# Optimization experiments

Measured on AMD Instinct MI355X. Metric: run time of the kernel, lower is better.

Reference implementation:

```python
import jax, jax.numpy as jnp
import numpy as np

NU, NI, F, H, D = 100000, 50000, 256, 8, 64
E1, E2 = 300000, 300000
SLOPE = 0.2  # DGL GATConv default negative_slope


def setup_inputs() -> dict:
    key = jax.random.key(0)
    ks = jax.random.split(key, 20)
    p = lambda k, sh: jax.random.normal(k, sh, jnp.float32) * 0.1
    return {
        "h_user": jax.random.normal(ks[0], (NU, F), jnp.float32),
        "h_item": jax.random.normal(ks[1], (NI, F), jnp.float32),
        "src_u2i": jax.random.randint(ks[2], (E1,), 0, NU),
        "dst_u2i": jax.random.randint(ks[3], (E1,), 0, NI),
        "src_i2u": jax.random.randint(ks[4], (E2,), 0, NI),
        "dst_i2u": jax.random.randint(ks[5], (E2,), 0, NU),
        "W_src_u2i": p(ks[6], (F, H * D)), "W_dst_u2i": p(ks[7], (F, H * D)),
        "al_u2i": p(ks[8], (H, D)), "ar_u2i": p(ks[9], (H, D)),
        "bias_u2i": jnp.zeros((H * D,), jnp.float32), "W_res_u2i": p(ks[10], (F, H * D)),
        "W_src_i2u": p(ks[11], (F, H * D)), "W_dst_i2u": p(ks[12], (F, H * D)),
        "al_i2u": p(ks[13], (H, D)), "ar_i2u": p(ks[14], (H, D)),
        "bias_i2u": jnp.zeros((H * D,), jnp.float32), "W_res_i2u": p(ks[15], (F, H * D)),
    }


def _gat(h_src, h_dst, src, dst, Ws, Wd, al, ar, b, Wr, n_dst):
    # linear projections -> [N, H, D]
    fs = (h_src @ Ws).reshape(-1, H, D)
    fd = (h_dst @ Wd).reshape(-1, H, D)
    el = jnp.einsum('nhd,hd->nh', fs, al)   # a_l . Wh_src
    er = jnp.einsum('nhd,hd->nh', fd, ar)   # a_r . Wh_dst
    e = jax.nn.leaky_relu(el[src] + er[dst], SLOPE)  # [E, H]
    # segment softmax over incoming edges of each dst node
    m = jax.ops.segment_max(e, dst, num_segments=n_dst)
    m = jnp.where(jnp.isfinite(m), m, jnp.float32(0))  # nodes with no edges
    ex = jnp.exp(e - m[dst])
    s = jax.ops.segment_sum(ex, dst, num_segments=n_dst)
    a = ex / s[dst]                                   # [E, H]
    # weighted scatter-sum of gathered source features
    out = jax.ops.segment_sum(a[:, :, None] * fs[src], dst, num_segments=n_dst)
    res = (h_dst @ Wr).reshape(-1, H, D)              # residual projection
    return out + res + b.reshape(1, H, D)


def reference(h_user, h_item, src_u2i, dst_u2i, src_i2u, dst_i2u,
              W_src_u2i, W_dst_u2i, al_u2i, ar_u2i, bias_u2i, W_res_u2i,
              W_src_i2u, W_dst_i2u, al_i2u, ar_i2u, bias_i2u, W_res_i2u):
    out_item = _gat(h_user, h_item, src_u2i, dst_u2i,
                    W_src_u2i, W_dst_u2i, al_u2i, ar_u2i, bias_u2i, W_res_u2i, NI)
    out_user = _gat(h_item, h_user, src_i2u, dst_i2u,
                    W_src_i2u, W_dst_i2u, al_i2u, ar_i2u, bias_i2u, W_res_i2u, NU)
    return (out_user, out_item)
```

## Files before the change

### kernel.cpp

```cpp
#include <hip/hip_runtime.h>
#include <cstdint>
#include <cstddef>

#define NU_ 100000
#define NI_ 50000
#define F_ 256
#define H_ 8
#define HD_ 512
#define NE_ 300000
#define SLOPE_ 0.2f

#define MPAD_U 100096
#define MPAD_I 50048
#define MT_U (MPAD_U / 128)
#define MT_I (MPAD_I / 128)
#define GEMM_NB ((MT_U + MT_I) * 4)

#define SCAN_N (NI_ + NU_)
#define SCAN_CHUNK 2048
#define SCAN_NB ((SCAN_N + SCAN_CHUNK - 1) / SCAN_CHUNK)

#define PREP_COPY_U (NU_ * F_ / 2048)
#define PREP_COPY_I (NI_ * F_ / 2048)
#define PREP_COPY (PREP_COPY_U + PREP_COPY_I)
#define PREP_WCONV 2048
#define PREP_FOLD 32
#define PREP_HIST ((2 * NE_ + 255) / 256)
#define PREP_NB (PREP_COPY + PREP_WCONV + PREP_FOLD + PREP_HIST)

typedef float f32x4 __attribute__((ext_vector_type(4)));
typedef __bf16 bf16x8 __attribute__((ext_vector_type(8)));
typedef unsigned short u16x8 __attribute__((ext_vector_type(8)));
typedef unsigned short u16x4 __attribute__((ext_vector_type(4)));

static __device__ __forceinline__ unsigned short f2bf_bits(float f) {
  unsigned u = __float_as_uint(f);
  u += 0x7fffu + ((u >> 16) & 1u);
  return (unsigned short)(u >> 16);
}
static __device__ __forceinline__ float bf2f(unsigned short b) {
  return __uint_as_float(((unsigned)b) << 16);
}
static __device__ __forceinline__ unsigned cvt_pk_bf16(float lo, float hi) {
  unsigned r;
  asm("v_cvt_pk_bf16_f32 %0, %1, %2" : "=v"(r) : "v"(lo), "v"(hi));
  return r;
}

#define GLL16(g, l)                                                        \
  __builtin_amdgcn_global_load_lds(                                        \
      (const __attribute__((address_space(1))) void*)(g),                  \
      (__attribute__((address_space(3))) void*)(l), 16, 0, 0)

__global__ __launch_bounds__(256) void prep_kernel(const float* __restrict__ h_user,
                                                   const float* __restrict__ h_item,
                                                   const float* __restrict__ W0,
                                                   const float* __restrict__ W1,
                                                   const float* __restrict__ W2,
                                                   const float* __restrict__ W3,
                                                   const float* __restrict__ Wd0,
                                                   const float* __restrict__ Wd1,
                                                   const float* __restrict__ a0,
                                                   const float* __restrict__ a1,
                                                   const float* __restrict__ a2,
                                                   const float* __restrict__ a3,
                                                   const int* __restrict__ dst_u2i,
                                                   const int* __restrict__ dst_i2u,
                                                   unsigned short* __restrict__ hb_user,
                                                   unsigned short* __restrict__ hb_item,
                                                   unsigned short* __restrict__ Wt,
                                                   unsigned short* __restrict__ wfb,
                                                   int* __restrict__ deg) {
  int bid = blockIdx.x;
  if (bid < PREP_COPY) {
    bool user = bid < PREP_COPY_U;
    const float* h = user ? h_user : h_item;
    unsigned short* hb = user ? hb_user : hb_item;
    size_t base = (size_t)(user ? bid : bid - PREP_COPY_U) * 2048 + threadIdx.x * 8;
    f32x4 a = *(const f32x4*)&h[base];
    f32x4 b = *(const f32x4*)&h[base + 4];
    u16x8 o;
    o[0] = f2bf_bits(a.x); o[1] = f2bf_bits(a.y); o[2] = f2bf_bits(a.z); o[3] = f2bf_bits(a.w);
    o[4] = f2bf_bits(b.x); o[5] = f2bf_bits(b.y); o[6] = f2bf_bits(b.z); o[7] = f2bf_bits(b.w);
    *(u16x8*)&hb[base] = o;
  } else if (bid < PREP_COPY + PREP_WCONV) {
    int idx = (bid - PREP_COPY) * 256 + threadIdx.x;
    int m = idx >> 17;
    int r = idx & 131071;
    const float* W = (m == 0) ? W0 : (m == 1) ? W1 : (m == 2) ? W2 : W3;
    int f = r & 255, c = r >> 8;
    Wt[idx] = f2bf_bits(W[(size_t)f * HD_ + c]);
  } else if (bid < PREP_COPY + PREP_WCONV + PREP_FOLD) {
    int b = bid - PREP_COPY - PREP_WCONV;
    int m = b >> 3;
    int idx = (b & 7) * 256 + threadIdx.x;
    const float* W = (m == 0) ? W0 : (m == 1) ? Wd0 : (m == 2) ? W2 : Wd1;
    const float* av = (m == 0) ? a0 : (m == 1) ? a1 : (m == 2) ? a2 : a3;
    int f = idx & 255, hh = idx >> 8;
    float acc = 0.f;
#pragma unroll 8
    for (int d = 0; d < 64; ++d) acc += W[(size_t)f * HD_ + hh * 64 + d] * av[hh * 64 + d];
    int buf = (m == 0 || m == 3) ? 0 : 1;
    int rowoff = (m == 1 || m == 3) ? 8 : 0;
    wfb[buf * 4096 + (rowoff + hh) * 256 + f] = f2bf_bits(acc);
  } else {
    int e = (bid - PREP_COPY - PREP_WCONV - PREP_FOLD) * 256 + threadIdx.x;
    if (e < NE_) atomicAdd(&deg[dst_u2i[e]], 1);
    else if (e < 2 * NE_) atomicAdd(&deg[NI_ + dst_i2u[e - NE_]], 1);
  }
}

__global__ __launch_bounds__(256) void gemm2_kernel(const unsigned short* __restrict__ hb_user,
                                                    const unsigned short* __restrict__ hb_item,
                                                    const unsigned short* __restrict__ Wt,
                                                    const unsigned short* __restrict__ wfb,
                                                    unsigned short* __restrict__ fs_u2i,
                                                    unsigned short* __restrict__ fs_i2u,
                                                    unsigned short* __restrict__ res_user,
                                                    unsigned short* __restrict__ res_item,
                                                    const float* __restrict__ bias_u2i,
                                                    const float* __restrict__ bias_i2u,
                                                    float* __restrict__ el_u2i,
                                                    float* __restrict__ er_i2u,
                                                    float* __restrict__ el_i2u,
                                                    float* __restrict__ er_u2i,
                                                    const int* __restrict__ deg,
                                                    int* __restrict__ bsum) {
  __shared__ unsigned short lds[2][3][128][32];
  if (blockIdx.x >= GEMM_NB) {
    int* ilds = (int*)&lds[0][0][0][0];
    int tid = threadIdx.x;
    int base = (blockIdx.x - GEMM_NB) * SCAN_CHUNK + tid * 8;
    int sum = 0;
#pragma unroll
    for (int j = 0; j < 8; ++j) sum += (base + j < SCAN_N) ? deg[base + j] : 0;
    ilds[tid] = sum;
    __syncthreads();
    for (int o = 128; o > 0; o >>= 1) {
      if (tid < o) ilds[tid] += ilds[tid + o];
      __syncthreads();
    }
    if (tid == 0) bsum[blockIdx.x - GEMM_NB] = ilds[0];
    return;
  }
  int bid;
  {
    constexpr int qq = GEMM_NB / 8, rr = GEMM_NB % 8;
    int xcd = blockIdx.x & 7, sidx = blockIdx.x >> 3;
    bid = (xcd < rr ? xcd * (qq + 1) : rr * (qq + 1) + (xcd - rr) * qq) + sidx;
  }
  bool user = bid < MT_U * 4;
  if (!user) bid -= MT_U * 4;
  const unsigned short* Ab  = user ? hb_user : hb_item;
  const unsigned short* B1t = user ? (Wt + 0 * HD_ * F_) : (Wt + 2 * HD_ * F_);
  const unsigned short* B2t = user ? (Wt + 3 * HD_ * F_) : (Wt + 1 * HD_ * F_);
  const unsigned short* wfs = user ? wfb : (wfb + 4096);
  unsigned short* fs  = user ? fs_u2i : fs_i2u;
  unsigned short* res = user ? res_user : res_item;
  const float* bias = user ? bias_i2u : bias_u2i;
  int M = user ? NU_ : NI_;

  int tid = threadIdx.x;
  int lane = tid & 63;
  int wave = tid >> 6;
  int wm = wave >> 1, wn = wave & 1;
  int mt = bid >> 2, nt = bid & 3;
  int bm = mt * 128, bn = nt * 128;
  f32x4 acc1[4][4] = {};
  f32x4 acc2[4][4] = {};
  f32x4 acc3[4] = {};
  int lr = lane & 15;
  int kk = (lane >> 4) * 8;
  int ksw = ((lane >> 4) ^ ((lr >> 1) & 3)) << 3;

  int r0 = tid >> 2;
  int c0 = (tid & 3) << 3;
  int cs = (((tid & 3) ^ ((r0 >> 1) & 3)) << 3);
  const unsigned short* gA  = &Ab [(size_t)(bm + r0) * 256 + cs];
  const unsigned short* gB1 = &B1t[(size_t)(bn + r0) * 256 + cs];
  const unsigned short* gB2 = &B2t[(size_t)(bn + r0) * 256 + cs];

  bf16x8 b3f[8];
  if (nt == 0) {
#pragma unroll
    for (int t = 0; t < 8; ++t)
      b3f[t] = __builtin_bit_cast(bf16x8, *(const u16x8*)&wfs[(size_t)lr * 256 + kk + t * 32]);
  }

#define STAGE(buf, t)                                                       \
  do {                                                                      \
    int k0_ = (t) * 32;                                                     \
    GLL16(gA  + k0_,          &lds[buf][0][r0][c0]);                        \
    GLL16(gA  + k0_ + 64*256, &lds[buf][0][r0 + 64][c0]);                   \
    GLL16(gB1 + k0_,          &lds[buf][1][r0][c0]);                        \
    GLL16(gB1 + k0_ + 64*256, &lds[buf][1][r0 + 64][c0]);                   \
    GLL16(gB2 + k0_,          &lds[buf][2][r0][c0]);                        \
    GLL16(gB2 + k0_ + 64*256, &lds[buf][2][r0 + 64][c0]);                   \
  } while (0)

  STAGE(0, 0);
#pragma unroll
  for (int t = 0; t < 8; ++t) {
    if (t < 7) STAGE((t + 1) & 1, t + 1);
    if (t < 7) asm volatile("s_waitcnt vmcnt(6)" ::: "memory");
    else       asm volatile("s_waitcnt vmcnt(0)" ::: "memory");
    __builtin_amdgcn_s_barrier();
    __builtin_amdgcn_sched_barrier(0);
    const int cb = t & 1;
    bf16x8 af[4], b1[4], b2[4];
#pragma unroll
    for (int m = 0; m < 4; ++m)
      af[m] = __builtin_bit_cast(bf16x8, *(const u16x8*)&lds[cb][0][wm * 64 + m * 16 + lr][ksw]);
#pragma unroll
    for (int n = 0; n < 4; ++n) {
      b1[n] = __builtin_bit_cast(bf16x8, *(const u16x8*)&lds[cb][1][wn * 64 + n * 16 + lr][ksw]);
      b2[n] = __builtin_bit_cast(bf16x8, *(const u16x8*)&lds[cb][2][wn * 64 + n * 16 + lr][ksw]);
    }
#pragma unroll
    for (int m = 0; m < 4; ++m)
#pragma unroll
      for (int n = 0; n < 4; ++n) {
        acc1[m][n] = __builtin_amdgcn_mfma_f32_16x16x32_bf16(b1[n], af[m], acc1[m][n], 0, 0, 0);
        acc2[m][n] = __builtin_amdgcn_mfma_f32_16x16x32_bf16(b2[n], af[m], acc2[m][n], 0, 0, 0);
      }
    if (nt == 0) {
#pragma unroll
      for (int m = 0; m < 4; ++m)
        acc3[m] = __builtin_amdgcn_mfma_f32_16x16x32_bf16(af[m], b3f[t], acc3[m], 0, 0, 0);
    }
    __builtin_amdgcn_sched_barrier(0);
    __builtin_amdgcn_s_barrier();
  }
#undef STAGE

  int rg = (lane >> 4) * 4;
  f32x4 bsv[4];
#pragma unroll
  for (int n = 0; n < 4; ++n)
    bsv[n] = *(const f32x4*)&bias[bn + wn * 64 + n * 16 + rg];
#pragma unroll
  for (int m = 0; m < 4; ++m) {
    int row = bm + wm * 64 + m * 16 + lr;
    if (row < M) {
#pragma unroll
      for (int n = 0; n < 4; ++n) {
        int col = bn + wn * 64 + n * 16 + rg;
        uint2 v1;
        v1.x = cvt_pk_bf16(acc1[m][n][0], acc1[m][n][1]);
        v1.y = cvt_pk_bf16(acc1[m][n][2], acc1[m][n][3]);
        *(uint2*)&fs[(size_t)row * HD_ + col] = v1;
        uint2 v2;
        v2.x = cvt_pk_bf16(acc2[m][n][0] + bsv[n].x, acc2[m][n][1] + bsv[n].y);
        v2.y = cvt_pk_bf16(acc2[m][n][2] + bsv[n].z, acc2[m][n][3] + bsv[n].w);
        *(uint2*)&res[(size_t)row * HD_ + col] = v2;
      }
    }
  }
  if (nt == 0 && wn == 0) {
    float* elp = user ? el_u2i : el_i2u;
    float* erp = user ? er_i2u : er_u2i;
#pragma unroll
    for (int m = 0; m < 4; ++m) {
#pragma unroll
      for (int r = 0; r < 4; ++r) {
        int row = bm + wm * 64 + m * 16 + rg + r;
        if (row >= M) continue;
        if (lr < 8) elp[(size_t)row * 8 + lr] = acc3[m][r];
        else        erp[(size_t)row * 8 + lr - 8] = acc3[m][r];
      }
    }
  }
}

__global__ __launch_bounds__(256) void scan_apply_kernel(const int* __restrict__ deg,
                                                         const int* __restrict__ bsum,
                                                         int* __restrict__ rowstart,
                                                         int* __restrict__ cursor) {
  __shared__ int sb[128];
  __shared__ int lds[256];
  int tid = threadIdx.x;
  if (tid < 128) sb[tid] = (tid < SCAN_NB) ? bsum[tid] : 0;
  __syncthreads();
  for (int o = 1; o < 128; o <<= 1) {
    int t = (tid < 128 && tid >= o) ? sb[tid - o] : 0;
    __syncthreads();
    if (tid < 128) sb[tid] += t;
    __syncthreads();
  }
  int blockpref = (blockIdx.x == 0) ? 0 : sb[blockIdx.x - 1];
  int base = blockIdx.x * SCAN_CHUNK + tid * 8;
  int v[8];
  int sum = 0;
#pragma unroll
  for (int j = 0; j < 8; ++j) {
    v[j] = (base + j < SCAN_N) ? deg[base + j] : 0;
    sum += v[j];
  }
  lds[tid] = sum;
  __syncthreads();
  for (int o = 1; o < 256; o <<= 1) {
    int t = (tid >= o) ? lds[tid - o] : 0;
    __syncthreads();
    lds[tid] += t;
    __syncthreads();
  }
  int run = blockpref + lds[tid] - sum;
#pragma unroll
  for (int j = 0; j < 8; ++j) {
    if (base + j < SCAN_N) { rowstart[base + j] = run; cursor[base + j] = run; }
    run += v[j];
  }
  if (blockIdx.x == 0 && tid == 0) rowstart[SCAN_N] = 2 * NE_;
}

__global__ __launch_bounds__(256) void bin_kernel(const int* __restrict__ src_u2i,
                                                  const int* __restrict__ dst_u2i,
                                                  const int* __restrict__ src_i2u,
                                                  const int* __restrict__ dst_i2u,
                                                  int* __restrict__ cursor,
                                                  int* __restrict__ ssrc) {
  int e = blockIdx.x * 256 + threadIdx.x;
  int de, se;
  if (e < NE_) { de = dst_u2i[e]; se = src_u2i[e]; }
  else if (e < 2 * NE_) { de = NI_ + dst_i2u[e - NE_]; se = src_i2u[e - NE_]; }
  else return;
  int pos = atomicAdd(&cursor[de], 1);
  ssrc[pos] = se;
}

__global__ __launch_bounds__(256) void accum_kernel(const int* __restrict__ rowstart,
                                                    const int* __restrict__ ssrc,
                                                    const float* __restrict__ el_u2i,
                                                    const float* __restrict__ el_i2u,
                                                    const float* __restrict__ er_u2i,
                                                    const float* __restrict__ er_i2u,
                                                    const unsigned short* __restrict__ fs_u2i,
                                                    const unsigned short* __restrict__ fs_i2u,
                                                    const unsigned short* __restrict__ res_user,
                                                    const unsigned short* __restrict__ res_item,
                                                    float* __restrict__ out_item,
                                                    float* __restrict__ out_user) {
  int n = blockIdx.x * 4 + (threadIdx.x >> 6);
  int lane = threadIdx.x & 63;
  bool item = n < NI_;
  int ln = item ? n : n - NI_;
  const unsigned short* res = item ? res_item : res_user;
  float* out = (item ? out_item : out_user) + (size_t)ln * HD_;
  int r0 = rowstart[n], r1 = rowstart[n + 1];
  float acc[8] = {};
  if (r0 < r1) {
    const float* el = item ? el_u2i : el_i2u;
    const float* er = item ? er_u2i : er_i2u;
    const unsigned short* fs = item ? fs_u2i : fs_i2u;
    int hh = lane >> 3;
    float erh = er[(size_t)ln * 8 + hh];
    float m = -3.0e38f, s = 0.f;
    int k = r0;
    for (; k + 2 <= r1; k += 2) {
      int s0 = ssrc[k], s1 = ssrc[k + 1];
      float e0 = el[(size_t)s0 * 8 + hh] + erh;
      float e1 = el[(size_t)s1 * 8 + hh] + erh;
      e0 = e0 > 0.f ? e0 : SLOPE_ * e0;
      e1 = e1 > 0.f ? e1 : SLOPE_ * e1;
      u16x8 v0 = *(const u16x8*)&fs[(size_t)s0 * HD_ + lane * 8];
      u16x8 v1 = *(const u16x8*)&fs[(size_t)s1 * HD_ + lane * 8];
      float mm = fmaxf(e0, e1);
      if (mm > m) {
        float r = __expf(m - mm);
        s *= r;
#pragma unroll
        for (int j = 0; j < 8; ++j) acc[j] *= r;
        m = mm;
      }
      float x0 = __expf(e0 - m), x1 = __expf(e1 - m);
      s += x0 + x1;
#pragma unroll
      for (int j = 0; j < 8; ++j)
        acc[j] += x0 * bf2f((unsigned short)v0[j]) + x1 * bf2f((unsigned short)v1[j]);
    }
    if (k < r1) {
      int s0 = ssrc[k];
      float e0 = el[(size_t)s0 * 8 + hh] + erh;
      e0 = e0 > 0.f ? e0 : SLOPE_ * e0;
      u16x8 v0 = *(const u16x8*)&fs[(size_t)s0 * HD_ + lane * 8];
      if (e0 > m) {
        float r = __expf(m - e0);
        s *= r;
#pragma unroll
        for (int j = 0; j < 8; ++j) acc[j] *= r;
        m = e0;
      }
      float x0 = __expf(e0 - m);
      s += x0;
#pragma unroll
      for (int j = 0; j < 8; ++j) acc[j] += x0 * bf2f((unsigned short)v0[j]);
    }
    float inv = 1.f / s;
#pragma unroll
    for (int j = 0; j < 8; ++j) acc[j] *= inv;
  }
  u16x8 rv = *(const u16x8*)&res[(size_t)ln * HD_ + lane * 8];
  f32x4 o0, o1;
#pragma unroll
  for (int j = 0; j < 4; ++j) {
    o0[j] = acc[j] + bf2f((unsigned short)rv[j]);
    o1[j] = acc[4 + j] + bf2f((unsigned short)rv[4 + j]);
  }
  float* op = out + lane * 8;
  *(f32x4*)op = o0;
  *(f32x4*)(op + 4) = o1;
}

extern "C" void kernel_launch(void* const* d_in, const int* in_sizes, int n_in,
                              void* d_out, int out_size, void* d_ws, size_t ws_size,
                              hipStream_t stream) {
  const float* h_user    = (const float*)d_in[0];
  const float* h_item    = (const float*)d_in[1];
  const int*   src_u2i   = (const int*)d_in[2];
  const int*   dst_u2i   = (const int*)d_in[3];
  const int*   src_i2u   = (const int*)d_in[4];
  const int*   dst_i2u   = (const int*)d_in[5];
  const float* W_src_u2i = (const float*)d_in[6];
  const float* W_dst_u2i = (const float*)d_in[7];
  const float* al_u2i    = (const float*)d_in[8];
  const float* ar_u2i    = (const float*)d_in[9];
  const float* bias_u2i  = (const float*)d_in[10];
  const float* W_res_u2i = (const float*)d_in[11];
  const float* W_src_i2u = (const float*)d_in[12];
  const float* W_dst_i2u = (const float*)d_in[13];
  const float* al_i2u    = (const float*)d_in[14];
  const float* ar_i2u    = (const float*)d_in[15];
  const float* bias_i2u  = (const float*)d_in[16];
  const float* W_res_i2u = (const float*)d_in[17];

  float* out_user = (float*)d_out;
  float* out_item = (float*)d_out + (size_t)NU_ * HD_;

  char* ws = (char*)d_ws;
  size_t off = 0;
  auto take = [&](size_t bytes) -> char* {
    char* p = ws + off;
    off += (bytes + 255) & ~(size_t)255;
    return p;
  };
  unsigned short* fs_u2i   = (unsigned short*)take((size_t)NU_ * HD_ * 2);
  unsigned short* fs_i2u   = (unsigned short*)take((size_t)NI_ * HD_ * 2);
  unsigned short* res_user = (unsigned short*)take((size_t)NU_ * HD_ * 2);
  unsigned short* res_item = (unsigned short*)take((size_t)NI_ * HD_ * 2);
  unsigned short* hb_user  = (unsigned short*)take((size_t)MPAD_U * F_ * 2);
  unsigned short* hb_item  = (unsigned short*)take((size_t)MPAD_I * F_ * 2);
  unsigned short* Wt  = (unsigned short*)take((size_t)4 * HD_ * F_ * 2);
  unsigned short* wfb = (unsigned short*)take((size_t)2 * 16 * F_ * 2);
  float* el_u2i = (float*)take((size_t)NU_ * 8 * 4);
  float* er_i2u = (float*)take((size_t)NU_ * 8 * 4);
  float* el_i2u = (float*)take((size_t)NI_ * 8 * 4);
  float* er_u2i = (float*)take((size_t)NI_ * 8 * 4);
  int* deg_all      = (int*)take((size_t)SCAN_N * 4);
  int* rowstart_all = (int*)take((size_t)(SCAN_N + 1) * 4);
  int* cursor_all   = (int*)take((size_t)SCAN_N * 4);
  int* bsum         = (int*)take((size_t)128 * 4);
  int* ssrc         = (int*)take((size_t)2 * NE_ * 4);

  hipMemsetAsync(deg_all, 0, (size_t)SCAN_N * 4, stream);

  prep_kernel<<<PREP_NB, 256, 0, stream>>>(h_user, h_item,
                                           W_src_u2i, W_res_u2i, W_src_i2u, W_res_i2u,
                                           W_dst_u2i, W_dst_i2u,
                                           al_u2i, ar_u2i, al_i2u, ar_i2u,
                                           dst_u2i, dst_i2u,
                                           hb_user, hb_item, Wt, wfb, deg_all);

  gemm2_kernel<<<GEMM_NB + SCAN_NB, 256, 0, stream>>>(hb_user, hb_item, Wt, wfb,
                                                      fs_u2i, fs_i2u, res_user, res_item,
                                                      bias_u2i, bias_i2u,
                                                      el_u2i, er_i2u, el_i2u, er_u2i,
                                                      deg_all, bsum);

  scan_apply_kernel<<<SCAN_NB, 256, 0, stream>>>(deg_all, bsum, rowstart_all, cursor_all);
  constexpr int EB2 = (2 * NE_ + 255) / 256;
  bin_kernel<<<EB2, 256, 0, stream>>>(src_u2i, dst_u2i, src_i2u, dst_i2u, cursor_all, ssrc);

  accum_kernel<<<SCAN_N / 4, 256, 0, stream>>>(rowstart_all, ssrc,
                                               el_u2i, el_i2u, er_u2i, er_i2u,
                                               fs_u2i, fs_i2u, res_user, res_item,
                                               out_item, out_user);
}
```

Measured before the change: 498.0 us.

## Split dual-output GEMM into single-output tiles with separate el/er blocks and LDS-staged stores

Each GEMM block previously computed both the source projection and the residual projection for one A tile, with the attention-logit MFMA folded in. Now each block computes one output (fs or res), so there are twice as many blocks. Each block uses two LDS operands instead of three and holds half the accumulators, which should cut register pressure and raise occupancy. The el/er logits move into dedicated blocks that read A directly from global memory, and the epilogue stages bf16 results through padded LDS so the global stores are coalesced 16-byte writes. The cost is that each A tile is loaded twice from memory, plus one more time by the el/er blocks.

Measured after the change: 462.5 us (median of 4 runs). 1.08x faster.

```diff
diff --git a/kernel.cpp b/kernel.cpp
--- a/kernel.cpp
+++ b/kernel.cpp
@@ -14,7 +14,8 @@
 #define MPAD_I 50048
 #define MT_U (MPAD_U / 128)
 #define MT_I (MPAD_I / 128)
-#define GEMM_NB ((MT_U + MT_I) * 4)
+#define NT_ALL ((MT_U + MT_I) * 8)
+#define EL_NB (MT_U + MT_I)
 
 #define SCAN_N (NI_ + NU_)
 #define SCAN_CHUNK 2048
@@ -32,6 +33,7 @@
 typedef __bf16 bf16x8 __attribute__((ext_vector_type(8)));
 typedef unsigned short u16x8 __attribute__((ext_vector_type(8)));
 typedef unsigned short u16x4 __attribute__((ext_vector_type(4)));
+typedef unsigned int u32x4 __attribute__((ext_vector_type(4)));
 
 static __device__ __forceinline__ unsigned short f2bf_bits(float f) {
   unsigned u = __float_as_uint(f);
@@ -110,6 +112,8 @@
   }
 }
 
+#define EPITCH 136
+#define LOFF(b, m, r) ((((b) * 2 + (m)) * 128 + (r)) * 32)
 __global__ __launch_bounds__(256) void gemm2_kernel(const unsigned short* __restrict__ hb_user,
                                                     const unsigned short* __restrict__ hb_item,
                                                     const unsigned short* __restrict__ Wt,
@@ -126,11 +130,16 @@
                                                     float* __restrict__ er_u2i,
                                                     const int* __restrict__ deg,
                                                     int* __restrict__ bsum) {
-  __shared__ unsigned short lds[2][3][128][32];
-  if (blockIdx.x >= GEMM_NB) {
-    int* ilds = (int*)&lds[0][0][0][0];
-    int tid = threadIdx.x;
-    int base = (blockIdx.x - GEMM_NB) * SCAN_CHUNK + tid * 8;
+  __shared__ unsigned short sh[17408];
+  int tid = threadIdx.x;
+  int lane = tid & 63;
+  int wave = tid >> 6;
+  int lr = lane & 15;
+  int kk = (lane >> 4) * 8;
+
+  if (blockIdx.x >= NT_ALL + EL_NB) {
+    int* ilds = (int*)sh;
+    int base = (blockIdx.x - NT_ALL - EL_NB) * SCAN_CHUNK + tid * 8;
     int sum = 0;
 #pragma unroll
     for (int j = 0; j < 8; ++j) sum += (base + j < SCAN_N) ? deg[base + j] : 0;
@@ -140,137 +149,146 @@
       if (tid < o) ilds[tid] += ilds[tid + o];
       __syncthreads();
     }
-    if (tid == 0) bsum[blockIdx.x - GEMM_NB] = ilds[0];
+    if (tid == 0) bsum[blockIdx.x - NT_ALL - EL_NB] = ilds[0];
     return;
   }
-  int bid;
-  {
-    constexpr int qq = GEMM_NB / 8, rr = GEMM_NB % 8;
-    int xcd = blockIdx.x & 7, sidx = blockIdx.x >> 3;
-    bid = (xcd < rr ? xcd * (qq + 1) : rr * (qq + 1) + (xcd - rr) * qq) + sidx;
-  }
-  bool user = bid < MT_U * 4;
-  if (!user) bid -= MT_U * 4;
-  const unsigned short* Ab  = user ? hb_user : hb_item;
-  const unsigned short* B1t = user ? (Wt + 0 * HD_ * F_) : (Wt + 2 * HD_ * F_);
-  const unsigned short* B2t = user ? (Wt + 3 * HD_ * F_) : (Wt + 1 * HD_ * F_);
-  const unsigned short* wfs = user ? wfb : (wfb + 4096);
-  unsigned short* fs  = user ? fs_u2i : fs_i2u;
-  unsigned short* res = user ? res_user : res_item;
-  const float* bias = user ? bias_i2u : bias_u2i;
-  int M = user ? NU_ : NI_;
-
-  int tid = threadIdx.x;
-  int lane = tid & 63;
-  int wave = tid >> 6;
-  int wm = wave >> 1, wn = wave & 1;
-  int mt = bid >> 2, nt = bid & 3;
-  int bm = mt * 128, bn = nt * 128;
-  f32x4 acc1[4][4] = {};
-  f32x4 acc2[4][4] = {};
-  f32x4 acc3[4] = {};
-  int lr = lane & 15;
-  int kk = (lane >> 4) * 8;
-  int ksw = ((lane >> 4) ^ ((lr >> 1) & 3)) << 3;
-
-  int r0 = tid >> 2;
-  int c0 = (tid & 3) << 3;
-  int cs = (((tid & 3) ^ ((r0 >> 1) & 3)) << 3);
-  const unsigned short* gA  = &Ab [(size_t)(bm + r0) * 256 + cs];
-  const unsigned short* gB1 = &B1t[(size_t)(bn + r0) * 256 + cs];
-  const unsigned short* gB2 = &B2t[(size_t)(bn + r0) * 256 + cs];
-
-  bf16x8 b3f[8];
-  if (nt == 0) {
-#pragma unroll
-    for (int t = 0; t < 8; ++t)
-      b3f[t] = __builtin_bit_cast(bf16x8, *(const u16x8*)&wfs[(size_t)lr * 256 + kk + t * 32]);
-  }
-
-#define STAGE(buf, t)                                                       \
-  do {                                                                      \
-    int k0_ = (t) * 32;                                                     \
-    GLL16(gA  + k0_,          &lds[buf][0][r0][c0]);                        \
-    GLL16(gA  + k0_ + 64*256, &lds[buf][0][r0 + 64][c0]);                   \
-    GLL16(gB1 + k0_,          &lds[buf][1][r0][c0]);                        \
-    GLL16(gB1 + k0_ + 64*256, &lds[buf][1][r0 + 64][c0]);                   \
-    GLL16(gB2 + k0_,          &lds[buf][2][r0][c0]);                        \
-    GLL16(gB2 + k0_ + 64*256, &lds[buf][2][r0 + 64][c0]);                   \
-  } while (0)
-
-  STAGE(0, 0);
-#pragma unroll
-  for (int t = 0; t < 8; ++t) {
-    if (t < 7) STAGE((t + 1) & 1, t + 1);
-    if (t < 7) asm volatile("s_waitcnt vmcnt(6)" ::: "memory");
-    else       asm volatile("s_waitcnt vmcnt(0)" ::: "memory");
-    __builtin_amdgcn_s_barrier();
-    __builtin_amdgcn_sched_barrier(0);
-    const int cb = t & 1;
-    bf16x8 af[4], b1[4], b2[4];
-#pragma unroll
-    for (int m = 0; m < 4; ++m)
-      af[m] = __builtin_bit_cast(bf16x8, *(const u16x8*)&lds[cb][0][wm * 64 + m * 16 + lr][ksw]);
-#pragma unroll
-    for (int n = 0; n < 4; ++n) {
-      b1[n] = __builtin_bit_cast(bf16x8, *(const u16x8*)&lds[cb][1][wn * 64 + n * 16 + lr][ksw]);
-      b2[n] = __builtin_bit_cast(bf16x8, *(const u16x8*)&lds[cb][2][wn * 64 + n * 16 + lr][ksw]);
-    }
-#pragma unroll
-    for (int m = 0; m < 4; ++m)
-#pragma unroll
-      for (int n = 0; n < 4; ++n) {
-        acc1[m][n] = __builtin_amdgcn_mfma_f32_16x16x32_bf16(b1[n], af[m], acc1[m][n], 0, 0, 0);
-        acc2[m][n] = __builtin_amdgcn_mfma_f32_16x16x32_bf16(b2[n], af[m], acc2[m][n], 0, 0, 0);
-      }
-    if (nt == 0) {
-#pragma unroll
-      for (int m = 0; m < 4; ++m)
-        acc3[m] = __builtin_amdgcn_mfma_f32_16x16x32_bf16(af[m], b3f[t], acc3[m], 0, 0, 0);
-    }
-    __builtin_amdgcn_sched_barrier(0);
-    __builtin_amdgcn_s_barrier();
-  }
-#undef STAGE
-
-  int rg = (lane >> 4) * 4;
-  f32x4 bsv[4];
-#pragma unroll
-  for (int n = 0; n < 4; ++n)
-    bsv[n] = *(const f32x4*)&bias[bn + wn * 64 + n * 16 + rg];
-#pragma unroll
-  for (int m = 0; m < 4; ++m) {
-    int row = bm + wm * 64 + m * 16 + lr;
-    if (row < M) {
-#pragma unroll
-      for (int n = 0; n < 4; ++n) {
-        int col = bn + wn * 64 + n * 16 + rg;
-        uint2 v1;
-        v1.x = cvt_pk_bf16(acc1[m][n][0], acc1[m][n][1]);
-        v1.y = cvt_pk_bf16(acc1[m][n][2], acc1[m][n][3]);
-        *(uint2*)&fs[(size_t)row * HD_ + col] = v1;
-        uint2 v2;
-        v2.x = cvt_pk_bf16(acc2[m][n][0] + bsv[n].x, acc2[m][n][1] + bsv[n].y);
-        v2.y = cvt_pk_bf16(acc2[m][n][2] + bsv[n].z, acc2[m][n][3] + bsv[n].w);
-        *(uint2*)&res[(size_t)row * HD_ + col] = v2;
+
+  if (blockIdx.x >= NT_ALL) {
+    int mt = blockIdx.x - NT_ALL;
+    bool user = mt < MT_U;
+    int lm = user ? mt : mt - MT_U;
+    const unsigned short* A = user ? hb_user : hb_item;
+    const unsigned short* wfs = user ? wfb : (wfb + 4096);
+    float* elp = user ? el_u2i : el_i2u;
+    float* erp = user ? er_i2u : er_u2i;
+    int M = user ? NU_ : NI_;
+    int bm = lm * 128;
+    int mf0 = wave * 2;
+    f32x4 acc3[2] = {};
+#pragma unroll
+    for (int t = 0; t < 8; ++t) {
+      int ko = kk + t * 32;
+      bf16x8 b3 = __builtin_bit_cast(bf16x8, *(const u16x8*)&wfs[(size_t)lr * 256 + ko]);
+#pragma unroll
+      for (int m = 0; m < 2; ++m) {
+        bf16x8 af = __builtin_bit_cast(
+            bf16x8, *(const u16x8*)&A[(size_t)(bm + (mf0 + m) * 16 + lr) * 256 + ko]);
+        acc3[m] = __builtin_amdgcn_mfma_f32_16x16x32_bf16(af, b3, acc3[m], 0, 0, 0);
       }
     }
-  }
-  if (nt == 0 && wn == 0) {
-    float* elp = user ? el_u2i : el_i2u;
-    float* erp = user ? er_i2u : er_u2i;
-#pragma unroll
-    for (int m = 0; m < 4; ++m) {
+    int rg = (lane >> 4) * 4;
+#pragma unroll
+    for (int m = 0; m < 2; ++m) {
 #pragma unroll
       for (int r = 0; r < 4; ++r) {
-        int row = bm + wm * 64 + m * 16 + rg + r;
+        int row = bm + (mf0 + m) * 16 + rg + r;
         if (row >= M) continue;
         if (lr < 8) elp[(size_t)row * 8 + lr] = acc3[m][r];
         else        erp[(size_t)row * 8 + lr - 8] = acc3[m][r];
       }
     }
-  }
-}
+    return;
+  }
+
+  int bid;
+  {
+    constexpr int qq = NT_ALL / 8;
+    bid = (blockIdx.x & 7) * qq + (blockIdx.x >> 3);
+  }
+  bool user = bid < MT_U * 8;
+  int b = user ? bid : bid - MT_U * 8;
+  int mt = b >> 3;
+  int sub = b & 7;
+  int nt = sub >> 1;
+  bool isres = sub & 1;
+  const unsigned short* Ab = user ? hb_user : hb_item;
+  const unsigned short* Bt = user ? (isres ? Wt + 3 * HD_ * F_ : Wt + 0 * HD_ * F_)
+                                  : (isres ? Wt + 1 * HD_ * F_ : Wt + 2 * HD_ * F_);
+  unsigned short* dst = user ? (isres ? res_user : fs_u2i)
+                             : (isres ? res_item : fs_i2u);
+  const float* bias = user ? bias_i2u : bias_u2i;
+  int M = user ? NU_ : NI_;
+
+  int wm = wave >> 1, wn = wave & 1;
+  int bm = mt * 128, bn = nt * 128;
+  f32x4 acc[4][4] = {};
+  int ksw = ((lane >> 4) ^ ((lr >> 1) & 3)) << 3;
+
+  int r0 = tid >> 2;
+  int c0 = (tid & 3) << 3;
+  int cs = (((tid & 3) ^ ((r0 >> 1) & 3)) << 3);
+  const unsigned short* gA = &Ab[(size_t)(bm + r0) * 256 + cs];
+  const unsigned short* gB = &Bt[(size_t)(bn + r0) * 256 + cs];
+
+#define STAGE(buf, t)                                                       \
+  do {                                                                      \
+    int k0_ = (t) * 32;                                                     \
+    GLL16(gA + k0_,            &sh[LOFF(buf, 0, r0) + c0]);                 \
+    GLL16(gA + k0_ + 64 * 256, &sh[LOFF(buf, 0, r0 + 64) + c0]);            \
+    GLL16(gB + k0_,            &sh[LOFF(buf, 1, r0) + c0]);                 \
+    GLL16(gB + k0_ + 64 * 256, &sh[LOFF(buf, 1, r0 + 64) + c0]);            \
+  } while (0)
+
+  STAGE(0, 0);
+#pragma unroll
+  for (int t = 0; t < 8; ++t) {
+    if (t < 7) STAGE((t + 1) & 1, t + 1);
+    if (t < 7) asm volatile("s_waitcnt vmcnt(4)" ::: "memory");
+    else       asm volatile("s_waitcnt vmcnt(0)" ::: "memory");
+    __builtin_amdgcn_s_barrier();
+    __builtin_amdgcn_sched_barrier(0);
+    const int cb = t & 1;
+    bf16x8 af[4], bf[4];
+#pragma unroll
+    for (int m = 0; m < 4; ++m)
+      af[m] = __builtin_bit_cast(bf16x8,
+          *(const u16x8*)&sh[LOFF(cb, 0, wm * 64 + m * 16 + lr) + ksw]);
+#pragma unroll
+    for (int n = 0; n < 4; ++n)
+      bf[n] = __builtin_bit_cast(bf16x8,
+          *(const u16x8*)&sh[LOFF(cb, 1, wn * 64 + n * 16 + lr) + ksw]);
+#pragma unroll
+    for (int m = 0; m < 4; ++m)
+#pragma unroll
+      for (int n = 0; n < 4; ++n)
+        acc[m][n] = __builtin_amdgcn_mfma_f32_16x16x32_bf16(bf[n], af[m], acc[m][n], 0, 0, 0);
+    __builtin_amdgcn_sched_barrier(0);
+    __builtin_amdgcn_s_barrier();
+  }
+#undef STAGE
+
+  int rg = (lane >> 4) * 4;
+  f32x4 bsv[4];
+#pragma unroll
+  for (int n = 0; n < 4; ++n) {
+    if (isres) bsv[n] = *(const f32x4*)&bias[bn + wn * 64 + n * 16 + rg];
+    else       bsv[n] = f32x4{0.f, 0.f, 0.f, 0.f};
+  }
+
+  __syncthreads();
+#pragma unroll
+  for (int m = 0; m < 4; ++m) {
+    int rowl = wm * 64 + m * 16 + lr;
+#pragma unroll
+    for (int n = 0; n < 4; ++n) {
+      int coll = wn * 64 + n * 16 + rg;
+      uint2 v;
+      v.x = cvt_pk_bf16(acc[m][n][0] + bsv[n].x, acc[m][n][1] + bsv[n].y);
+      v.y = cvt_pk_bf16(acc[m][n][2] + bsv[n].z, acc[m][n][3] + bsv[n].w);
+      *(uint2*)&sh[rowl * EPITCH + coll] = v;
+    }
+  }
+  __syncthreads();
+#pragma unroll
+  for (int p = 0; p < 8; ++p) {
+    int id = tid + p * 256;
+    int rowl = id >> 4, c16 = (id & 15) * 8;
+    int growl = bm + rowl;
+    if (growl < M)
+      *(u32x4*)&dst[(size_t)growl * HD_ + bn + c16] = *(const u32x4*)&sh[rowl * EPITCH + c16];
+  }
+}
+#undef LOFF
 
 __global__ __launch_bounds__(256) void scan_apply_kernel(const int* __restrict__ deg,
                                                          const int* __restrict__ bsum,
@@ -470,11 +488,12 @@
                                            dst_u2i, dst_i2u,
                                            hb_user, hb_item, Wt, wfb, deg_all);
 
-  gemm2_kernel<<<GEMM_NB + SCAN_NB, 256, 0, stream>>>(hb_user, hb_item, Wt, wfb,
-                                                      fs_u2i, fs_i2u, res_user, res_item,
-                                                      bias_u2i, bias_i2u,
-                                                      el_u2i, er_i2u, el_i2u, er_u2i,
-                                                      deg_all, bsum);
+  gemm2_kernel<<<NT_ALL + EL_NB + SCAN_NB, 256, 0, stream>>>(
+      hb_user, hb_item, Wt, wfb,
+      fs_u2i, fs_i2u, res_user, res_item,
+      bias_u2i, bias_i2u,
+      el_u2i, er_i2u, el_i2u, er_u2i,
+      deg_all, bsum);
 
   scan_apply_kernel<<<SCAN_NB, 256, 0, stream>>>(deg_all, bsum, rowstart_all, cursor_all);
   constexpr int EB2 = (2 * NE_ + 255) / 256;
```
